# Performance work log

Hardware: AMD Instinct MI355X
Metric: run time of the kernel (lower is better)

The kernel has to match this reference:

```python
import jax, jax.numpy as jnp
import numpy as np
import math

B, V, J, F, N = 32, 25000, 20, 50000, 200000
MIN_SCALE, MAX_SCALE = 5e-4, 0.05
INIT_SCALE = 0.005
EPS = 1e-8


def _normalize(x):
    return x / jnp.sqrt(jnp.sum(x * x, -1, keepdims=True) + 1e-12)


def _rodrigues(aa):
    # aa: [..., 3] axis-angle -> [..., 3, 3] rotation matrix
    theta = jnp.sqrt(jnp.sum(aa * aa, -1, keepdims=True) + 1e-12)
    axis = aa / theta
    x, y, z = axis[..., 0], axis[..., 1], axis[..., 2]
    zero = jnp.zeros_like(x)
    K = jnp.stack([zero, -z, y, z, zero, -x, -y, x, zero], -1).reshape(aa.shape[:-1] + (3, 3))
    s = jnp.sin(theta)[..., None]
    c = jnp.cos(theta)[..., None]
    I = jnp.eye(3, dtype=aa.dtype)
    return I + s * K + (1.0 - c) * (K @ K)


def _rt_to_mat4(R, t):
    top = jnp.concatenate([R, t[..., :, None]], axis=-1)  # [...,3,4]
    bot = jnp.broadcast_to(jnp.array([0.0, 0.0, 0.0, 1.0], R.dtype), top.shape[:-2] + (1, 4))
    return jnp.concatenate([top, bot], axis=-2)


def _rot_to_quat(R):
    # wxyz convention, branchless version of the torch masked code
    r00, r01, r02 = R[..., 0, 0], R[..., 0, 1], R[..., 0, 2]
    r10, r11, r12 = R[..., 1, 0], R[..., 1, 1], R[..., 1, 2]
    r20, r21, r22 = R[..., 2, 0], R[..., 2, 1], R[..., 2, 2]
    tr = r00 + r11 + r22
    s1 = jnp.sqrt(jnp.maximum(tr + 1.0, EPS)) * 2
    q1 = jnp.stack([0.25 * s1, (r21 - r12) / s1, (r02 - r20) / s1, (r10 - r01) / s1], -1)
    s2 = jnp.sqrt(jnp.maximum(1.0 + r00 - r11 - r22, EPS)) * 2
    q2 = jnp.stack([(r21 - r12) / s2, 0.25 * s2, (r01 + r10) / s2, (r02 + r20) / s2], -1)
    s3 = jnp.sqrt(jnp.maximum(1.0 + r11 - r00 - r22, EPS)) * 2
    q3 = jnp.stack([(r02 - r20) / s3, (r01 + r10) / s3, 0.25 * s3, (r12 + r21) / s3], -1)
    s4 = jnp.sqrt(jnp.maximum(1.0 + r22 - r00 - r11, EPS)) * 2
    q4 = jnp.stack([(r10 - r01) / s4, (r02 + r20) / s4, (r12 + r21) / s4, 0.25 * s4], -1)
    m1 = (tr > 0)[..., None]
    m2 = ((tr <= 0) & (r00 > r11) & (r00 > r22))[..., None]
    m3 = ((tr <= 0) & ~((r00 > r11) & (r00 > r22)) & (r11 > r22))[..., None]
    q = jnp.where(m1, q1, jnp.where(m2, q2, jnp.where(m3, q3, q4)))
    return _normalize(q)


def _quat_mul(a, b):
    # Hamilton product, wxyz
    w1, x1, y1, z1 = a[..., 0], a[..., 1], a[..., 2], a[..., 3]
    w2, x2, y2, z2 = b[..., 0], b[..., 1], b[..., 2], b[..., 3]
    return jnp.stack([
        w1 * w2 - x1 * x2 - y1 * y2 - z1 * z2,
        w1 * x2 + x1 * w2 + y1 * z2 - z1 * y2,
        w1 * y2 - x1 * z2 + y1 * w2 + z1 * x2,
        w1 * z2 + x1 * y2 - y1 * x2 + z1 * w2,
    ], -1)


def setup_inputs() -> dict:
    key = jax.random.key(0)
    ks = jax.random.split(key, 12)
    pose = 0.3 * jax.random.normal(ks[0], (B, J * 3), jnp.float32)
    trans = jax.random.normal(ks[1], (B, 3), jnp.float32)
    scale = 0.75 + 0.5 * jax.random.uniform(ks[2], (B, 1), jnp.float32)
    v_template = jax.random.normal(ks[3], (V, 3), jnp.float32)
    w = jax.random.uniform(ks[4], (V, J), jnp.float32) + 1e-3
    skin_weights = w / jnp.sum(w, -1, keepdims=True)
    joints_rest = jax.random.normal(ks[5], (J, 3), jnp.float32)
    position_offsets = 0.001 * jax.random.normal(ks[6], (N, 3), jnp.float32)
    colors_raw = 0.1 * jax.random.normal(ks[7], (N, 3), jnp.float32) - 1.7
    opacity_raw = jnp.full((N,), math.log(0.9 / 0.1), jnp.float32)
    log_scales = math.log(INIT_SCALE) + 0.1 * jax.random.normal(ks[8], (N, 3), jnp.float32)
    quaternions = jnp.concatenate(
        [jnp.ones((N, 1), jnp.float32), 0.01 * jax.random.normal(ks[9], (N, 3), jnp.float32)], -1)
    vertex_indices = jax.random.randint(ks[10], (N,), 0, V, jnp.int32)
    faces = jax.random.randint(ks[11], (F, 3), 0, V, jnp.int32)
    return dict(pose=pose, trans=trans, scale=scale, v_template=v_template,
                skin_weights=skin_weights, joints_rest=joints_rest,
                position_offsets=position_offsets, colors_raw=colors_raw,
                opacity_raw=opacity_raw, log_scales=log_scales,
                quaternions=quaternions, vertex_indices=vertex_indices, faces=faces)


def _lbs_vertices(pose, trans, scale, v_template, skin_weights, joints_rest):
    b = pose.shape[0]
    R = _rodrigues(pose.reshape(b, J, 3))  # [B,J,3,3]
    # kinematic chain: joint j's parent is j-1, joint 0 is root
    G = _rt_to_mat4(R[:, 0], jnp.broadcast_to(joints_rest[0], (b, 3)))
    Gs = [G]
    for j in range(1, J):
        L = _rt_to_mat4(R[:, j], jnp.broadcast_to(joints_rest[j] - joints_rest[j - 1], (b, 3)))
        G = G @ L
        Gs.append(G)
    G = jnp.stack(Gs, 1)  # [B,J,4,4]
    Rg = G[..., :3, :3]
    tg = G[..., :3, 3] - jnp.einsum('bjxy,jy->bjx', Rg, joints_rest)  # remove rest-pose joint
    A = _rt_to_mat4(Rg, tg)  # [B,J,4,4] relative transforms
    T = jnp.einsum('vj,bjxy->bvxy', skin_weights, A)  # blended per-vertex transform
    Vp = jnp.einsum('bvxy,vy->bvx', T[..., :3, :3], v_template) + T[..., :3, 3]
    return Vp * scale[:, None, :] + trans[:, None, :]  # [B,V,3]


def _tangent_frames(Vw, faces):
    fv = Vw[:, faces]  # [B,F,3,3]
    fn = jnp.cross(fv[:, :, 1] - fv[:, :, 0], fv[:, :, 2] - fv[:, :, 0])  # [B,F,3]
    nrm = jnp.zeros_like(Vw)
    for k in range(3):
        nrm = nrm.at[:, faces[:, k]].add(fn)
    n = _normalize(nrm)
    ref = jnp.where(jnp.abs(n[..., 0:1]) < 0.9,
                    jnp.array([1.0, 0.0, 0.0], n.dtype), jnp.array([0.0, 0.0, 1.0], n.dtype))
    t = _normalize(ref - jnp.sum(ref * n, -1, keepdims=True) * n)
    bt = jnp.cross(n, t)
    return n, t, bt


def reference(pose, trans, scale, v_template, skin_weights, joints_rest,
              position_offsets, colors_raw, opacity_raw, log_scales, quaternions,
              vertex_indices, faces):
    b = pose.shape[0]
    Vw = _lbs_vertices(pose, trans, scale, v_template, skin_weights, joints_rest)
    base = Vw[:, vertex_indices]  # [B,N,3] gather
    n, t, bt = _tangent_frames(Vw, faces)
    Ng = n[:, vertex_indices]
    Tg = t[:, vertex_indices]
    Bg = bt[:, vertex_indices]
    off = position_offsets[None]
    means = base + off[..., 0:1] * Tg + off[..., 1:2] * Bg + off[..., 2:3] * Ng
    frame = jnp.stack([Tg, Bg, Ng], axis=-1)  # [B,N,3,3] columns = T,B,N
    fq = _rot_to_quat(frame)
    lq = _normalize(quaternions)
    rotations = _quat_mul(fq, jnp.broadcast_to(lq[None], fq.shape))
    colors = jnp.broadcast_to(jax.nn.sigmoid(colors_raw)[None], (b, N, 3))
    opacity = jnp.broadcast_to(jax.nn.sigmoid(opacity_raw)[None], (b, N))
    scales = jnp.broadcast_to(jnp.clip(jnp.exp(log_scales), MIN_SCALE, MAX_SCALE)[None], (b, N, 3))
    return means, colors, opacity, scales, rotations
```

## Files before the change

### kernel.cpp

```cpp
#include <hip/hip_runtime.h>
#include <math.h>

namespace {
constexpr int kB = 32;
constexpr int kV = 25000;
constexpr int kJ = 20;
constexpr int kF = 50000;
constexpr int kN = 200000;
constexpr int kCap = 40;

constexpr float kEps = 1e-8f;

constexpr size_t OFF_MEANS  = 0;
constexpr size_t OFF_COLORS = (size_t)kB * kN * 3;
constexpr size_t OFF_OPAC   = OFF_COLORS + (size_t)kB * kN * 3;
constexpr size_t OFF_SCALE  = OFF_OPAC + (size_t)kB * kN;
constexpr size_t OFF_ROT    = OFF_SCALE + (size_t)kB * kN * 3;


constexpr size_t WS_A   = 0;
constexpr size_t WS_CNT = 32768;
constexpr size_t WS_TRI = 135168;
}

__global__ void fill_bucket_kernel(const int* __restrict__ faces,
                                   int* __restrict__ cursor,
                                   int4* __restrict__ tri) {
    int f = blockIdx.x * blockDim.x + threadIdx.x;
    if (f >= kF) return;
    int i0 = faces[f * 3 + 0];
    int i1 = faces[f * 3 + 1];
    int i2 = faces[f * 3 + 2];
    int4 rec = make_int4(i0, i1, i2, 0);
#pragma unroll
    for (int k = 0; k < 3; ++k) {
        int v = (k == 0) ? i0 : (k == 1) ? i1 : i2;
        int p = atomicAdd(&cursor[v], 1);
        if (p < kCap) tri[(size_t)p * kV + v] = rec;
    }
}

__global__ void jt_kernel(const float* __restrict__ pose,
                          const float* __restrict__ jr,
                          float* __restrict__ A) {
    int b = threadIdx.x;
    if (b >= kB) return;

    float Gr[9], Gt[3];
    for (int j = 0; j < kJ; ++j) {
        float ax = pose[b * (kJ * 3) + j * 3 + 0];
        float ay = pose[b * (kJ * 3) + j * 3 + 1];
        float az = pose[b * (kJ * 3) + j * 3 + 2];
        float t2 = ax * ax + ay * ay + az * az + 1e-12f;
        float th = sqrtf(t2);
        float inv = 1.0f / th;
        float ux = ax * inv, uy = ay * inv, uz = az * inv;
        float s = sinf(th), c = cosf(th), oc = 1.0f - c;
        float R[9];
        R[0] = 1.0f + oc * (-(uy * uy + uz * uz));
        R[1] = -s * uz + oc * (ux * uy);
        R[2] =  s * uy + oc * (ux * uz);
        R[3] =  s * uz + oc * (ux * uy);
        R[4] = 1.0f + oc * (-(ux * ux + uz * uz));
        R[5] = -s * ux + oc * (uy * uz);
        R[6] = -s * uy + oc * (ux * uz);
        R[7] =  s * ux + oc * (uy * uz);
        R[8] = 1.0f + oc * (-(ux * ux + uy * uy));

        float jx = jr[j * 3 + 0], jy = jr[j * 3 + 1], jz = jr[j * 3 + 2];

        if (j == 0) {
            for (int k = 0; k < 9; ++k) Gr[k] = R[k];
            Gt[0] = jx; Gt[1] = jy; Gt[2] = jz;
        } else {
            float pjx = jr[(j - 1) * 3 + 0];
            float pjy = jr[(j - 1) * 3 + 1];
            float pjz = jr[(j - 1) * 3 + 2];
            float ltx = jx - pjx, lty = jy - pjy, ltz = jz - pjz;
            float nR[9], nT[3];
            for (int r = 0; r < 3; ++r) {
                float g0 = Gr[r * 3 + 0], g1 = Gr[r * 3 + 1], g2 = Gr[r * 3 + 2];
                nR[r * 3 + 0] = g0 * R[0] + g1 * R[3] + g2 * R[6];
                nR[r * 3 + 1] = g0 * R[1] + g1 * R[4] + g2 * R[7];
                nR[r * 3 + 2] = g0 * R[2] + g1 * R[5] + g2 * R[8];
                nT[r] = g0 * ltx + g1 * lty + g2 * ltz + Gt[r];
            }
            for (int k = 0; k < 9; ++k) Gr[k] = nR[k];
            Gt[0] = nT[0]; Gt[1] = nT[1]; Gt[2] = nT[2];
        }

        float tgx = Gt[0] - (Gr[0] * jx + Gr[1] * jy + Gr[2] * jz);
        float tgy = Gt[1] - (Gr[3] * jx + Gr[4] * jy + Gr[5] * jz);
        float tgz = Gt[2] - (Gr[6] * jx + Gr[7] * jy + Gr[8] * jz);
        float* Ao = A + ((size_t)b * kJ + j) * 12;
        Ao[0] = Gr[0]; Ao[1] = Gr[1]; Ao[2]  = Gr[2]; Ao[3]  = tgx;
        Ao[4] = Gr[3]; Ao[5] = Gr[4]; Ao[6]  = Gr[5]; Ao[7]  = tgy;
        Ao[8] = Gr[6]; Ao[9] = Gr[7]; Ao[10] = Gr[8]; Ao[11] = tgz;
    }
}

__global__ void skin_kernel(const float* __restrict__ A,
                            const float* __restrict__ sw,
                            const float* __restrict__ vt,
                            const float* __restrict__ scale,
                            const float* __restrict__ trans,
                            float4* __restrict__ Vw) {
    int b = blockIdx.y;
    int v = blockIdx.x * blockDim.x + threadIdx.x;
    __shared__ float sA[kJ * 12];
    if (threadIdx.x < kJ * 12) sA[threadIdx.x] = A[(size_t)b * kJ * 12 + threadIdx.x];
    __syncthreads();
    if (v >= kV) return;

    const float4* sw4 = (const float4*)(sw + (size_t)v * kJ);
    float w[kJ];
#pragma unroll
    for (int q = 0; q < 5; ++q) {
        float4 f = sw4[q];
        w[q * 4 + 0] = f.x; w[q * 4 + 1] = f.y;
        w[q * 4 + 2] = f.z; w[q * 4 + 3] = f.w;
    }

    float T[12];
#pragma unroll
    for (int k = 0; k < 12; ++k) T[k] = 0.0f;
#pragma unroll
    for (int j = 0; j < kJ; ++j) {
        float wj = w[j];
#pragma unroll
        for (int k = 0; k < 12; ++k) T[k] += wj * sA[j * 12 + k];
    }
    float x = vt[v * 3 + 0], y = vt[v * 3 + 1], z = vt[v * 3 + 2];
    float px = T[0] * x + T[1] * y + T[2]  * z + T[3];
    float py = T[4] * x + T[5] * y + T[6]  * z + T[7];
    float pz = T[8] * x + T[9] * y + T[10] * z + T[11];
    float s = scale[b];
    float tx = trans[b * 3 + 0], ty = trans[b * 3 + 1], tz = trans[b * 3 + 2];
    Vw[(size_t)b * kV + v] = make_float4(px * s + tx, py * s + ty, pz * s + tz, 0.0f);
}

__global__ void frame_kernel(const float4* __restrict__ Vw,
                             const int* __restrict__ cnt,
                             const int4* __restrict__ tri,
                             float4* __restrict__ rec) {
    int b = blockIdx.y;
    int v = blockIdx.x * blockDim.x + threadIdx.x;
    if (v >= kV) return;
    const float4* base = Vw + (size_t)b * kV;
    float4 me = base[v];

    int deg = min(cnt[v], kCap);
    float sx = 0.0f, sy = 0.0f, sz = 0.0f;
    for (int i = 0; i < deg; ++i) {
        int4 t = tri[(size_t)i * kV + v];
        float4 a  = base[t.x];
        float4 c1 = base[t.y];
        float4 c2 = base[t.z];
        float e1x = c1.x - a.x, e1y = c1.y - a.y, e1z = c1.z - a.z;
        float e2x = c2.x - a.x, e2y = c2.y - a.y, e2z = c2.z - a.z;
        sx += e1y * e2z - e1z * e2y;
        sy += e1z * e2x - e1x * e2z;
        sz += e1x * e2y - e1y * e2x;
    }

    float ninv = rsqrtf(sx * sx + sy * sy + sz * sz + 1e-12f);
    float nx = sx * ninv, ny = sy * ninv, nz = sz * ninv;

    bool small = fabsf(nx) < 0.9f;
    float refx = small ? 1.0f : 0.0f;
    float refz = small ? 0.0f : 1.0f;
    float d = refx * nx + refz * nz;
    float tx0 = refx - d * nx, ty0 = -d * ny, tz0 = refz - d * nz;
    float tinv = rsqrtf(tx0 * tx0 + ty0 * ty0 + tz0 * tz0 + 1e-12f);
    float tx = tx0 * tinv, ty = ty0 * tinv, tz = tz0 * tinv;

    float btx = ny * tz - nz * ty;
    float bty = nz * tx - nx * tz;
    float btz = nx * ty - ny * tx;

    float r00 = tx, r01 = btx, r02 = nx;
    float r10 = ty, r11 = bty, r12 = ny;
    float r20 = tz, r21 = btz, r22 = nz;
    float tr = r00 + r11 + r22;
    float q0, q1, q2, q3;
    if (tr > 0.0f) {
        float s = sqrtf(fmaxf(tr + 1.0f, kEps)) * 2.0f;
        q0 = 0.25f * s;
        q1 = (r21 - r12) / s;
        q2 = (r02 - r20) / s;
        q3 = (r10 - r01) / s;
    } else if (r00 > r11 && r00 > r22) {
        float s = sqrtf(fmaxf(1.0f + r00 - r11 - r22, kEps)) * 2.0f;
        q0 = (r21 - r12) / s;
        q1 = 0.25f * s;
        q2 = (r01 + r10) / s;
        q3 = (r02 + r20) / s;
    } else if (r11 > r22) {
        float s = sqrtf(fmaxf(1.0f + r11 - r00 - r22, kEps)) * 2.0f;
        q0 = (r02 - r20) / s;
        q1 = (r01 + r10) / s;
        q2 = 0.25f * s;
        q3 = (r12 + r21) / s;
    } else {
        float s = sqrtf(fmaxf(1.0f + r22 - r00 - r11, kEps)) * 2.0f;
        q0 = (r10 - r01) / s;
        q1 = (r02 + r20) / s;
        q2 = (r12 + r21) / s;
        q3 = 0.25f * s;
    }
    float qinv = rsqrtf(q0 * q0 + q1 * q1 + q2 * q2 + q3 * q3 + 1e-12f);
    q0 *= qinv; q1 *= qinv; q2 *= qinv; q3 *= qinv;

    size_t ro = ((size_t)b * kV + v) * 2;
    rec[ro + 0] = make_float4(me.x, me.y, me.z, 0.0f);
    rec[ro + 1] = make_float4(q0, q1, q2, q3);
}

__global__ void finalize_mr4_kernel(const float4* __restrict__ rec,
                                    const int* __restrict__ vidx,
                                    const float* __restrict__ poff,
                                    const float* __restrict__ quat,
                                    float* __restrict__ out) {
    int b = blockIdx.y;
    int qi = blockIdx.x * blockDim.x + threadIdx.x;
    if (qi >= kN / 4) return;
    int n0 = qi * 4;

    int4 vi = *(const int4*)(vidx + n0);
    const float4* rb = rec + (size_t)b * kV * 2;

    float4 p[4], fq[4];
    p[0] = rb[(size_t)vi.x * 2]; fq[0] = rb[(size_t)vi.x * 2 + 1];
    p[1] = rb[(size_t)vi.y * 2]; fq[1] = rb[(size_t)vi.y * 2 + 1];
    p[2] = rb[(size_t)vi.z * 2]; fq[2] = rb[(size_t)vi.z * 2 + 1];
    p[3] = rb[(size_t)vi.w * 2]; fq[3] = rb[(size_t)vi.w * 2 + 1];

    const float4* po = (const float4*)(poff + (size_t)n0 * 3);
    float4 oa = po[0], ob = po[1], oc = po[2];
    float off[4][3] = {{oa.x, oa.y, oa.z}, {oa.w, ob.x, ob.y},
                       {ob.z, ob.w, oc.x}, {oc.y, oc.z, oc.w}};

    const float4* lq4 = (const float4*)(quat + (size_t)n0 * 4);

    float m[4][3];
    float4 rotv[4];
#pragma unroll
    for (int k = 0; k < 4; ++k) {
        float w = fq[k].x, x = fq[k].y, y = fq[k].z, z = fq[k].w;
        float tx = 1.0f - 2.0f * (y * y + z * z);
        float ty = 2.0f * (x * y + w * z);
        float tz = 2.0f * (x * z - w * y);
        float btx = 2.0f * (x * y - w * z);
        float bty = 1.0f - 2.0f * (x * x + z * z);
        float btz = 2.0f * (y * z + w * x);
        float nx = 2.0f * (x * z + w * y);
        float ny = 2.0f * (y * z - w * x);
        float nz = 1.0f - 2.0f * (x * x + y * y);

        float o0 = off[k][0], o1 = off[k][1], o2 = off[k][2];
        m[k][0] = p[k].x + o0 * tx + o1 * btx + o2 * nx;
        m[k][1] = p[k].y + o0 * ty + o1 * bty + o2 * ny;
        m[k][2] = p[k].z + o0 * tz + o1 * btz + o2 * nz;

        float4 lq = lq4[k];
        float lw = lq.x, lx = lq.y, ly = lq.z, lz = lq.w;
        float linv = rsqrtf(lw * lw + lx * lx + ly * ly + lz * lz + 1e-12f);
        lw *= linv; lx *= linv; ly *= linv; lz *= linv;

        rotv[k] = make_float4(w * lw - x * lx - y * ly - z * lz,
                              w * lx + x * lw + y * lz - z * ly,
                              w * ly - x * lz + y * lw + z * lx,
                              w * lz + x * ly - y * lx + z * lw);
    }

    size_t bn0 = (size_t)b * kN + n0;
    float4* mo = (float4*)(out + OFF_MEANS + bn0 * 3);
    mo[0] = make_float4(m[0][0], m[0][1], m[0][2], m[1][0]);
    mo[1] = make_float4(m[1][1], m[1][2], m[2][0], m[2][1]);
    mo[2] = make_float4(m[2][2], m[3][0], m[3][1], m[3][2]);
    float4* ro = (float4*)(out + OFF_ROT + bn0 * 4);
    ro[0] = rotv[0]; ro[1] = rotv[1]; ro[2] = rotv[2]; ro[3] = rotv[3];
}

__device__ __forceinline__ float sigm(float x) {
    return 1.0f / (1.0f + __expf(-x));
}
__device__ __forceinline__ float eclip(float x) {
    return fminf(fmaxf(__expf(x), 0.0005f), 0.05f);
}

__global__ void finalize_cos_kernel(const float* __restrict__ craw,
                                    const float* __restrict__ oraw,
                                    const float* __restrict__ lsc,
                                    float* __restrict__ out) {
    int b = blockIdx.y;
    int q = blockIdx.x * blockDim.x + threadIdx.x;
    if (q >= kN / 4) return;
    int n0 = q * 4;

    const float4* cr4 = (const float4*)(craw + (size_t)n0 * 3);
    float4 ca = cr4[0], cb = cr4[1], cc = cr4[2];
    float4 ov = *(const float4*)(oraw + n0);
    const float4* ls4 = (const float4*)(lsc + (size_t)n0 * 3);
    float4 la = ls4[0], lb = ls4[1], lc = ls4[2];

    float4 sa = make_float4(sigm(ca.x), sigm(ca.y), sigm(ca.z), sigm(ca.w));
    float4 sb = make_float4(sigm(cb.x), sigm(cb.y), sigm(cb.z), sigm(cb.w));
    float4 sc = make_float4(sigm(cc.x), sigm(cc.y), sigm(cc.z), sigm(cc.w));
    float4 so = make_float4(sigm(ov.x), sigm(ov.y), sigm(ov.z), sigm(ov.w));
    float4 ea = make_float4(eclip(la.x), eclip(la.y), eclip(la.z), eclip(la.w));
    float4 eb = make_float4(eclip(lb.x), eclip(lb.y), eclip(lb.z), eclip(lb.w));
    float4 ec = make_float4(eclip(lc.x), eclip(lc.y), eclip(lc.z), eclip(lc.w));

    size_t bn0 = (size_t)b * kN + n0;
    float4* co = (float4*)(out + OFF_COLORS + bn0 * 3);
    co[0] = sa; co[1] = sb; co[2] = sc;
    *(float4*)(out + OFF_OPAC + bn0) = so;
    float4* sco = (float4*)(out + OFF_SCALE + bn0 * 3);
    sco[0] = ea; sco[1] = eb; sco[2] = ec;
}

extern "C" void kernel_launch(void* const* d_in, const int* in_sizes, int n_in,
                              void* d_out, int out_size, void* d_ws, size_t ws_size,
                              hipStream_t stream) {
    const float* pose  = (const float*)d_in[0];
    const float* trans = (const float*)d_in[1];
    const float* scale = (const float*)d_in[2];
    const float* vt    = (const float*)d_in[3];
    const float* sw    = (const float*)d_in[4];
    const float* jr    = (const float*)d_in[5];
    const float* poff  = (const float*)d_in[6];
    const float* craw  = (const float*)d_in[7];
    const float* oraw  = (const float*)d_in[8];
    const float* lsc   = (const float*)d_in[9];
    const float* quat  = (const float*)d_in[10];
    const int*   vidx  = (const int*)d_in[11];
    const int*   faces = (const int*)d_in[12];
    float* out = (float*)d_out;
    char* ws = (char*)d_ws;

    float* A   = (float*)(ws + WS_A);
    int*   cnt = (int*)(ws + WS_CNT);
    int4*  tri = (int4*)(ws + WS_TRI);

    float4* rec = (float4*)(out + OFF_OPAC);
    float4* Vw  = (float4*)(out + OFF_SCALE);

    dim3 gV((kV + 255) / 256, kB);
    dim3 gQ((kN / 4 + 255) / 256, kB);

    hipMemsetAsync(cnt, 0, kV * sizeof(int), stream);
    fill_bucket_kernel<<<(kF + 255) / 256, 256, 0, stream>>>(faces, cnt, tri);

    jt_kernel<<<1, 64, 0, stream>>>(pose, jr, A);
    skin_kernel<<<gV, 256, 0, stream>>>(A, sw, vt, scale, trans, Vw);

    frame_kernel<<<gV, 256, 0, stream>>>(Vw, cnt, tri, rec);

    finalize_mr4_kernel<<<gQ, 256, 0, stream>>>(rec, vidx, poff, quat, out);

    finalize_cos_kernel<<<gQ, 256, 0, stream>>>(craw, oraw, lsc, out);
}
```

Before: 302.7 us.

## Process multiple batch items per thread to reuse per-vertex and per-splat inputs

Each thread of the skin, frame and finalize kernels now handles several batch elements, a group of 4 or 8. Batch-invariant data is loaded once and reused across the group: skin weights, rest vertices, triangle adjacency records, vertex indices, offsets, local quaternions and the sigmoid/exp results. This cuts redundant global reads and transcendental work, and shrinks the grid. In exchange it raises register pressure and reduces the number of blocks, which may lower occupancy and latency hiding for the gather-heavy kernels.

```diff
diff --git a/kernel.cpp b/kernel.cpp
--- a/kernel.cpp
+++ b/kernel.cpp
@@ -16,7 +16,6 @@
 constexpr size_t OFF_OPAC   = OFF_COLORS + (size_t)kB * kN * 3;
 constexpr size_t OFF_SCALE  = OFF_OPAC + (size_t)kB * kN;
 constexpr size_t OFF_ROT    = OFF_SCALE + (size_t)kB * kN * 3;
-
 
 constexpr size_t WS_A   = 0;
 constexpr size_t WS_CNT = 32768;
@@ -99,16 +98,18 @@
     }
 }
 
-__global__ void skin_kernel(const float* __restrict__ A,
-                            const float* __restrict__ sw,
-                            const float* __restrict__ vt,
-                            const float* __restrict__ scale,
-                            const float* __restrict__ trans,
-                            float4* __restrict__ Vw) {
-    int b = blockIdx.y;
+template <int BG>
+__global__ void skin_bg_kernel(const float* __restrict__ A,
+                               const float* __restrict__ sw,
+                               const float* __restrict__ vt,
+                               const float* __restrict__ scale,
+                               const float* __restrict__ trans,
+                               float4* __restrict__ Vw) {
+    int bg0 = blockIdx.y * BG;
     int v = blockIdx.x * blockDim.x + threadIdx.x;
-    __shared__ float sA[kJ * 12];
-    if (threadIdx.x < kJ * 12) sA[threadIdx.x] = A[(size_t)b * kJ * 12 + threadIdx.x];
+    __shared__ float sA[BG * kJ * 12];
+    for (int i = threadIdx.x; i < BG * kJ * 12; i += blockDim.x)
+        sA[i] = A[(size_t)bg0 * kJ * 12 + i];
     __syncthreads();
     if (v >= kV) return;
 
@@ -120,120 +121,132 @@
         w[q * 4 + 0] = f.x; w[q * 4 + 1] = f.y;
         w[q * 4 + 2] = f.z; w[q * 4 + 3] = f.w;
     }
-
-    float T[12];
-#pragma unroll
-    for (int k = 0; k < 12; ++k) T[k] = 0.0f;
-#pragma unroll
-    for (int j = 0; j < kJ; ++j) {
-        float wj = w[j];
-#pragma unroll
-        for (int k = 0; k < 12; ++k) T[k] += wj * sA[j * 12 + k];
-    }
     float x = vt[v * 3 + 0], y = vt[v * 3 + 1], z = vt[v * 3 + 2];
-    float px = T[0] * x + T[1] * y + T[2]  * z + T[3];
-    float py = T[4] * x + T[5] * y + T[6]  * z + T[7];
-    float pz = T[8] * x + T[9] * y + T[10] * z + T[11];
-    float s = scale[b];
-    float tx = trans[b * 3 + 0], ty = trans[b * 3 + 1], tz = trans[b * 3 + 2];
-    Vw[(size_t)b * kV + v] = make_float4(px * s + tx, py * s + ty, pz * s + tz, 0.0f);
-}
-
-__global__ void frame_kernel(const float4* __restrict__ Vw,
-                             const int* __restrict__ cnt,
-                             const int4* __restrict__ tri,
-                             float4* __restrict__ rec) {
-    int b = blockIdx.y;
+
+#pragma unroll
+    for (int g = 0; g < BG; ++g) {
+        int b = bg0 + g;
+        const float* sAg = sA + g * kJ * 12;
+        float T[12];
+#pragma unroll
+        for (int k = 0; k < 12; ++k) T[k] = 0.0f;
+#pragma unroll
+        for (int j = 0; j < kJ; ++j) {
+            float wj = w[j];
+#pragma unroll
+            for (int k = 0; k < 12; ++k) T[k] += wj * sAg[j * 12 + k];
+        }
+        float px = T[0] * x + T[1] * y + T[2]  * z + T[3];
+        float py = T[4] * x + T[5] * y + T[6]  * z + T[7];
+        float pz = T[8] * x + T[9] * y + T[10] * z + T[11];
+        float s = scale[b];
+        float tx = trans[b * 3 + 0], ty = trans[b * 3 + 1], tz = trans[b * 3 + 2];
+        Vw[(size_t)b * kV + v] = make_float4(px * s + tx, py * s + ty, pz * s + tz, 0.0f);
+    }
+}
+
+template <int BG>
+__global__ void frame_bg_kernel(const float4* __restrict__ Vw,
+                                const int* __restrict__ cnt,
+                                const int4* __restrict__ tri,
+                                float4* __restrict__ rec) {
+    int bg0 = blockIdx.y * BG;
     int v = blockIdx.x * blockDim.x + threadIdx.x;
     if (v >= kV) return;
-    const float4* base = Vw + (size_t)b * kV;
-    float4 me = base[v];
+
+    float sx[BG], sy[BG], sz[BG];
+#pragma unroll
+    for (int g = 0; g < BG; ++g) { sx[g] = 0.0f; sy[g] = 0.0f; sz[g] = 0.0f; }
 
     int deg = min(cnt[v], kCap);
-    float sx = 0.0f, sy = 0.0f, sz = 0.0f;
     for (int i = 0; i < deg; ++i) {
         int4 t = tri[(size_t)i * kV + v];
-        float4 a  = base[t.x];
-        float4 c1 = base[t.y];
-        float4 c2 = base[t.z];
-        float e1x = c1.x - a.x, e1y = c1.y - a.y, e1z = c1.z - a.z;
-        float e2x = c2.x - a.x, e2y = c2.y - a.y, e2z = c2.z - a.z;
-        sx += e1y * e2z - e1z * e2y;
-        sy += e1z * e2x - e1x * e2z;
-        sz += e1x * e2y - e1y * e2x;
-    }
-
-    float ninv = rsqrtf(sx * sx + sy * sy + sz * sz + 1e-12f);
-    float nx = sx * ninv, ny = sy * ninv, nz = sz * ninv;
-
-    bool small = fabsf(nx) < 0.9f;
-    float refx = small ? 1.0f : 0.0f;
-    float refz = small ? 0.0f : 1.0f;
-    float d = refx * nx + refz * nz;
-    float tx0 = refx - d * nx, ty0 = -d * ny, tz0 = refz - d * nz;
-    float tinv = rsqrtf(tx0 * tx0 + ty0 * ty0 + tz0 * tz0 + 1e-12f);
-    float tx = tx0 * tinv, ty = ty0 * tinv, tz = tz0 * tinv;
-
-    float btx = ny * tz - nz * ty;
-    float bty = nz * tx - nx * tz;
-    float btz = nx * ty - ny * tx;
-
-    float r00 = tx, r01 = btx, r02 = nx;
-    float r10 = ty, r11 = bty, r12 = ny;
-    float r20 = tz, r21 = btz, r22 = nz;
-    float tr = r00 + r11 + r22;
-    float q0, q1, q2, q3;
-    if (tr > 0.0f) {
-        float s = sqrtf(fmaxf(tr + 1.0f, kEps)) * 2.0f;
-        q0 = 0.25f * s;
-        q1 = (r21 - r12) / s;
-        q2 = (r02 - r20) / s;
-        q3 = (r10 - r01) / s;
-    } else if (r00 > r11 && r00 > r22) {
-        float s = sqrtf(fmaxf(1.0f + r00 - r11 - r22, kEps)) * 2.0f;
-        q0 = (r21 - r12) / s;
-        q1 = 0.25f * s;
-        q2 = (r01 + r10) / s;
-        q3 = (r02 + r20) / s;
-    } else if (r11 > r22) {
-        float s = sqrtf(fmaxf(1.0f + r11 - r00 - r22, kEps)) * 2.0f;
-        q0 = (r02 - r20) / s;
-        q1 = (r01 + r10) / s;
-        q2 = 0.25f * s;
-        q3 = (r12 + r21) / s;
-    } else {
-        float s = sqrtf(fmaxf(1.0f + r22 - r00 - r11, kEps)) * 2.0f;
-        q0 = (r10 - r01) / s;
-        q1 = (r02 + r20) / s;
-        q2 = (r12 + r21) / s;
-        q3 = 0.25f * s;
-    }
-    float qinv = rsqrtf(q0 * q0 + q1 * q1 + q2 * q2 + q3 * q3 + 1e-12f);
-    q0 *= qinv; q1 *= qinv; q2 *= qinv; q3 *= qinv;
-
-    size_t ro = ((size_t)b * kV + v) * 2;
-    rec[ro + 0] = make_float4(me.x, me.y, me.z, 0.0f);
-    rec[ro + 1] = make_float4(q0, q1, q2, q3);
-}
-
-__global__ void finalize_mr4_kernel(const float4* __restrict__ rec,
-                                    const int* __restrict__ vidx,
-                                    const float* __restrict__ poff,
-                                    const float* __restrict__ quat,
-                                    float* __restrict__ out) {
-    int b = blockIdx.y;
+#pragma unroll
+        for (int g = 0; g < BG; ++g) {
+            const float4* base = Vw + (size_t)(bg0 + g) * kV;
+            float4 a  = base[t.x];
+            float4 c1 = base[t.y];
+            float4 c2 = base[t.z];
+            float e1x = c1.x - a.x, e1y = c1.y - a.y, e1z = c1.z - a.z;
+            float e2x = c2.x - a.x, e2y = c2.y - a.y, e2z = c2.z - a.z;
+            sx[g] += e1y * e2z - e1z * e2y;
+            sy[g] += e1z * e2x - e1x * e2z;
+            sz[g] += e1x * e2y - e1y * e2x;
+        }
+    }
+
+#pragma unroll
+    for (int g = 0; g < BG; ++g) {
+        int b = bg0 + g;
+        float4 me = Vw[(size_t)b * kV + v];
+
+        float ninv = rsqrtf(sx[g] * sx[g] + sy[g] * sy[g] + sz[g] * sz[g] + 1e-12f);
+        float nx = sx[g] * ninv, ny = sy[g] * ninv, nz = sz[g] * ninv;
+
+        bool small = fabsf(nx) < 0.9f;
+        float refx = small ? 1.0f : 0.0f;
+        float refz = small ? 0.0f : 1.0f;
+        float d = refx * nx + refz * nz;
+        float tx0 = refx - d * nx, ty0 = -d * ny, tz0 = refz - d * nz;
+        float tinv = rsqrtf(tx0 * tx0 + ty0 * ty0 + tz0 * tz0 + 1e-12f);
+        float tx = tx0 * tinv, ty = ty0 * tinv, tz = tz0 * tinv;
+
+        float btx = ny * tz - nz * ty;
+        float bty = nz * tx - nx * tz;
+        float btz = nx * ty - ny * tx;
+
+        float r00 = tx, r01 = btx, r02 = nx;
+        float r10 = ty, r11 = bty, r12 = ny;
+        float r20 = tz, r21 = btz, r22 = nz;
+        float tr = r00 + r11 + r22;
+        float q0, q1, q2, q3;
+        if (tr > 0.0f) {
+            float s = sqrtf(fmaxf(tr + 1.0f, kEps)) * 2.0f;
+            q0 = 0.25f * s;
+            q1 = (r21 - r12) / s;
+            q2 = (r02 - r20) / s;
+            q3 = (r10 - r01) / s;
+        } else if (r00 > r11 && r00 > r22) {
+            float s = sqrtf(fmaxf(1.0f + r00 - r11 - r22, kEps)) * 2.0f;
+            q0 = (r21 - r12) / s;
+            q1 = 0.25f * s;
+            q2 = (r01 + r10) / s;
+            q3 = (r02 + r20) / s;
+        } else if (r11 > r22) {
+            float s = sqrtf(fmaxf(1.0f + r11 - r00 - r22, kEps)) * 2.0f;
+            q0 = (r02 - r20) / s;
+            q1 = (r01 + r10) / s;
+            q2 = 0.25f * s;
+            q3 = (r12 + r21) / s;
+        } else {
+            float s = sqrtf(fmaxf(1.0f + r22 - r00 - r11, kEps)) * 2.0f;
+            q0 = (r10 - r01) / s;
+            q1 = (r02 + r20) / s;
+            q2 = (r12 + r21) / s;
+            q3 = 0.25f * s;
+        }
+        float qinv = rsqrtf(q0 * q0 + q1 * q1 + q2 * q2 + q3 * q3 + 1e-12f);
+        q0 *= qinv; q1 *= qinv; q2 *= qinv; q3 *= qinv;
+
+        size_t ro = ((size_t)b * kV + v) * 2;
+        rec[ro + 0] = make_float4(me.x, me.y, me.z, 0.0f);
+        rec[ro + 1] = make_float4(q0, q1, q2, q3);
+    }
+}
+
+template <int BG>
+__global__ void finalize_mr_bg_kernel(const float4* __restrict__ rec,
+                                      const int* __restrict__ vidx,
+                                      const float* __restrict__ poff,
+                                      const float* __restrict__ quat,
+                                      float* __restrict__ out) {
+    int bg0 = blockIdx.y * BG;
     int qi = blockIdx.x * blockDim.x + threadIdx.x;
     if (qi >= kN / 4) return;
     int n0 = qi * 4;
 
     int4 vi = *(const int4*)(vidx + n0);
-    const float4* rb = rec + (size_t)b * kV * 2;
-
-    float4 p[4], fq[4];
-    p[0] = rb[(size_t)vi.x * 2]; fq[0] = rb[(size_t)vi.x * 2 + 1];
-    p[1] = rb[(size_t)vi.y * 2]; fq[1] = rb[(size_t)vi.y * 2 + 1];
-    p[2] = rb[(size_t)vi.z * 2]; fq[2] = rb[(size_t)vi.z * 2 + 1];
-    p[3] = rb[(size_t)vi.w * 2]; fq[3] = rb[(size_t)vi.w * 2 + 1];
+    int vix[4] = {vi.x, vi.y, vi.z, vi.w};
 
     const float4* po = (const float4*)(poff + (size_t)n0 * 3);
     float4 oa = po[0], ob = po[1], oc = po[2];
@@ -241,45 +254,63 @@
                        {ob.z, ob.w, oc.x}, {oc.y, oc.z, oc.w}};
 
     const float4* lq4 = (const float4*)(quat + (size_t)n0 * 4);
-
-    float m[4][3];
-    float4 rotv[4];
+    float lqn[4][4];
 #pragma unroll
     for (int k = 0; k < 4; ++k) {
-        float w = fq[k].x, x = fq[k].y, y = fq[k].z, z = fq[k].w;
-        float tx = 1.0f - 2.0f * (y * y + z * z);
-        float ty = 2.0f * (x * y + w * z);
-        float tz = 2.0f * (x * z - w * y);
-        float btx = 2.0f * (x * y - w * z);
-        float bty = 1.0f - 2.0f * (x * x + z * z);
-        float btz = 2.0f * (y * z + w * x);
-        float nx = 2.0f * (x * z + w * y);
-        float ny = 2.0f * (y * z - w * x);
-        float nz = 1.0f - 2.0f * (x * x + y * y);
-
-        float o0 = off[k][0], o1 = off[k][1], o2 = off[k][2];
-        m[k][0] = p[k].x + o0 * tx + o1 * btx + o2 * nx;
-        m[k][1] = p[k].y + o0 * ty + o1 * bty + o2 * ny;
-        m[k][2] = p[k].z + o0 * tz + o1 * btz + o2 * nz;
-
         float4 lq = lq4[k];
-        float lw = lq.x, lx = lq.y, ly = lq.z, lz = lq.w;
-        float linv = rsqrtf(lw * lw + lx * lx + ly * ly + lz * lz + 1e-12f);
-        lw *= linv; lx *= linv; ly *= linv; lz *= linv;
-
-        rotv[k] = make_float4(w * lw - x * lx - y * ly - z * lz,
-                              w * lx + x * lw + y * lz - z * ly,
-                              w * ly - x * lz + y * lw + z * lx,
-                              w * lz + x * ly - y * lx + z * lw);
-    }
-
-    size_t bn0 = (size_t)b * kN + n0;
-    float4* mo = (float4*)(out + OFF_MEANS + bn0 * 3);
-    mo[0] = make_float4(m[0][0], m[0][1], m[0][2], m[1][0]);
-    mo[1] = make_float4(m[1][1], m[1][2], m[2][0], m[2][1]);
-    mo[2] = make_float4(m[2][2], m[3][0], m[3][1], m[3][2]);
-    float4* ro = (float4*)(out + OFF_ROT + bn0 * 4);
-    ro[0] = rotv[0]; ro[1] = rotv[1]; ro[2] = rotv[2]; ro[3] = rotv[3];
+        float linv = rsqrtf(lq.x * lq.x + lq.y * lq.y + lq.z * lq.z +
+                            lq.w * lq.w + 1e-12f);
+        lqn[k][0] = lq.x * linv; lqn[k][1] = lq.y * linv;
+        lqn[k][2] = lq.z * linv; lqn[k][3] = lq.w * linv;
+    }
+
+#pragma unroll
+    for (int g = 0; g < BG; ++g) {
+        int b = bg0 + g;
+        const float4* rb = rec + (size_t)b * kV * 2;
+
+        float4 p[4], fq[4];
+#pragma unroll
+        for (int k = 0; k < 4; ++k) {
+            p[k]  = rb[(size_t)vix[k] * 2];
+            fq[k] = rb[(size_t)vix[k] * 2 + 1];
+        }
+
+        float m[4][3];
+        float4 rotv[4];
+#pragma unroll
+        for (int k = 0; k < 4; ++k) {
+            float w = fq[k].x, x = fq[k].y, y = fq[k].z, z = fq[k].w;
+            float tx = 1.0f - 2.0f * (y * y + z * z);
+            float ty = 2.0f * (x * y + w * z);
+            float tz = 2.0f * (x * z - w * y);
+            float btx = 2.0f * (x * y - w * z);
+            float bty = 1.0f - 2.0f * (x * x + z * z);
+            float btz = 2.0f * (y * z + w * x);
+            float nx = 2.0f * (x * z + w * y);
+            float ny = 2.0f * (y * z - w * x);
+            float nz = 1.0f - 2.0f * (x * x + y * y);
+
+            float o0 = off[k][0], o1 = off[k][1], o2 = off[k][2];
+            m[k][0] = p[k].x + o0 * tx + o1 * btx + o2 * nx;
+            m[k][1] = p[k].y + o0 * ty + o1 * bty + o2 * ny;
+            m[k][2] = p[k].z + o0 * tz + o1 * btz + o2 * nz;
+
+            float lw = lqn[k][0], lx = lqn[k][1], ly = lqn[k][2], lz = lqn[k][3];
+            rotv[k] = make_float4(w * lw - x * lx - y * ly - z * lz,
+                                  w * lx + x * lw + y * lz - z * ly,
+                                  w * ly - x * lz + y * lw + z * lx,
+                                  w * lz + x * ly - y * lx + z * lw);
+        }
+
+        size_t bn0 = (size_t)b * kN + n0;
+        float4* mo = (float4*)(out + OFF_MEANS + bn0 * 3);
+        mo[0] = make_float4(m[0][0], m[0][1], m[0][2], m[1][0]);
+        mo[1] = make_float4(m[1][1], m[1][2], m[2][0], m[2][1]);
+        mo[2] = make_float4(m[2][2], m[3][0], m[3][1], m[3][2]);
+        float4* ro = (float4*)(out + OFF_ROT + bn0 * 4);
+        ro[0] = rotv[0]; ro[1] = rotv[1]; ro[2] = rotv[2]; ro[3] = rotv[3];
+    }
 }
 
 __device__ __forceinline__ float sigm(float x) {
@@ -289,11 +320,12 @@
     return fminf(fmaxf(__expf(x), 0.0005f), 0.05f);
 }
 
-__global__ void finalize_cos_kernel(const float* __restrict__ craw,
-                                    const float* __restrict__ oraw,
-                                    const float* __restrict__ lsc,
-                                    float* __restrict__ out) {
-    int b = blockIdx.y;
+template <int BG>
+__global__ void finalize_cos_bg_kernel(const float* __restrict__ craw,
+                                       const float* __restrict__ oraw,
+                                       const float* __restrict__ lsc,
+                                       float* __restrict__ out) {
+    int bg0 = blockIdx.y * BG;
     int q = blockIdx.x * blockDim.x + threadIdx.x;
     if (q >= kN / 4) return;
     int n0 = q * 4;
@@ -312,12 +344,16 @@
     float4 eb = make_float4(eclip(lb.x), eclip(lb.y), eclip(lb.z), eclip(lb.w));
     float4 ec = make_float4(eclip(lc.x), eclip(lc.y), eclip(lc.z), eclip(lc.w));
 
-    size_t bn0 = (size_t)b * kN + n0;
-    float4* co = (float4*)(out + OFF_COLORS + bn0 * 3);
-    co[0] = sa; co[1] = sb; co[2] = sc;
-    *(float4*)(out + OFF_OPAC + bn0) = so;
-    float4* sco = (float4*)(out + OFF_SCALE + bn0 * 3);
-    sco[0] = ea; sco[1] = eb; sco[2] = ec;
+#pragma unroll
+    for (int g = 0; g < BG; ++g) {
+        int b = bg0 + g;
+        size_t bn0 = (size_t)b * kN + n0;
+        float4* co = (float4*)(out + OFF_COLORS + bn0 * 3);
+        co[0] = sa; co[1] = sb; co[2] = sc;
+        *(float4*)(out + OFF_OPAC + bn0) = so;
+        float4* sco = (float4*)(out + OFF_SCALE + bn0 * 3);
+        sco[0] = ea; sco[1] = eb; sco[2] = ec;
+    }
 }
 
 extern "C" void kernel_launch(void* const* d_in, const int* in_sizes, int n_in,
@@ -346,18 +382,23 @@
     float4* rec = (float4*)(out + OFF_OPAC);
     float4* Vw  = (float4*)(out + OFF_SCALE);
 
-    dim3 gV((kV + 255) / 256, kB);
-    dim3 gQ((kN / 4 + 255) / 256, kB);
+    constexpr int BGv = 4;
+    constexpr int BGm = 4;
+    constexpr int BGc = 8;
+
+    dim3 gV((kV + 255) / 256, kB / BGv);
+    dim3 gM((kN / 4 + 255) / 256, kB / BGm);
+    dim3 gC((kN / 4 + 255) / 256, kB / BGc);
 
     hipMemsetAsync(cnt, 0, kV * sizeof(int), stream);
     fill_bucket_kernel<<<(kF + 255) / 256, 256, 0, stream>>>(faces, cnt, tri);
 
     jt_kernel<<<1, 64, 0, stream>>>(pose, jr, A);
-    skin_kernel<<<gV, 256, 0, stream>>>(A, sw, vt, scale, trans, Vw);
-
-    frame_kernel<<<gV, 256, 0, stream>>>(Vw, cnt, tri, rec);
-
-    finalize_mr4_kernel<<<gQ, 256, 0, stream>>>(rec, vidx, poff, quat, out);
-
-    finalize_cos_kernel<<<gQ, 256, 0, stream>>>(craw, oraw, lsc, out);
-}
+    skin_bg_kernel<BGv><<<gV, 256, 0, stream>>>(A, sw, vt, scale, trans, Vw);
+
+    frame_bg_kernel<BGv><<<gV, 256, 0, stream>>>(Vw, cnt, tri, rec);
+
+    finalize_mr_bg_kernel<BGm><<<gM, 256, 0, stream>>>(rec, vidx, poff, quat, out);
+
+    finalize_cos_bg_kernel<BGc><<<gC, 256, 0, stream>>>(craw, oraw, lsc, out);
+}
```

After: 375.9 us. +24.2%, slower.
